# Kernel tuning notes

Hardware: AMD Instinct MI355X
Metric: run time of the kernel (lower is better)

## Reference

```python
import jax, jax.numpy as jnp
import numpy as np

# ---- static config (matches init_kwargs) ----
B, N, DIM = 1, 2048, 1024
H, KVH, D = 16, 8, 64
GQ = H // KVH                 # grouped queries per kv head
WS = 64                       # sliding window size (causal, exact)
CBS, STRIDE = 32, 16          # compress block size / sliding stride
SEL_BLK, NSEL, NMEM = 32, 4, 1
NCB = N // STRIDE             # num compressed blocks (128)
NFB = N // SEL_BLK            # num fine blocks (64)
NCPF = SEL_BLK // STRIDE      # compressed blocks per fine block (2)
HID = CBS * D                 # compress MLP hidden (expand factor 1.0)
SCALE = D ** -0.5
THETA = 10000.0
NEG = -jnp.finfo(jnp.float32).max


def setup_inputs():
    key = jax.random.key(0)
    ks = jax.random.split(key, 16)
    s = 0.02
    r = lambda i, shape: jax.random.normal(ks[i], shape, jnp.float32) * s
    return {
        "inp": jax.random.normal(ks[0], (B, N, DIM), jnp.float32),
        "norm_g": jnp.ones((DIM,), jnp.float32),
        "Wqkv": r(1, (DIM, (H + 2 * KVH) * D)),
        "mem_kv": r(2, (2, KVH, NMEM, D)),
        "k_pos": r(3, (KVH, CBS, D)),
        "v_pos": r(4, (KVH, CBS, D)),
        "kW1": r(5, (CBS * D, HID)), "kb1": jnp.zeros((HID,), jnp.float32),
        "kW2": r(6, (HID, D)), "kb2": jnp.zeros((D,), jnp.float32),
        "vW1": r(7, (CBS * D, HID)), "vb1": jnp.zeros((HID,), jnp.float32),
        "vW2": r(8, (HID, D)), "vb2": jnp.zeros((D,), jnp.float32),
        "combW": r(9, (DIM, 3 * H)),
        "combB": jnp.tile(jnp.array([-2.0, -2.0, 2.0], jnp.float32), H),
        "Wout": r(10, (H * D, DIM)),
    }


def _rope(t):
    # lucidrains rotary-embedding-torch: interleaved adjacent-pair rotation
    inv_freq = 1.0 / (THETA ** (jnp.arange(0, D, 2, dtype=jnp.float32) / D))
    ang = jnp.arange(N, dtype=jnp.float32)[:, None] * inv_freq        # [N, D/2]
    cos = jnp.repeat(jnp.cos(ang), 2, axis=-1)                        # [N, D]
    sin = jnp.repeat(jnp.sin(ang), 2, axis=-1)
    t2 = t.reshape(*t.shape[:-1], D // 2, 2)
    rot = jnp.stack([-t2[..., 1], t2[..., 0]], axis=-1).reshape(t.shape)
    return t * cos + rot * sin


def _forward(inp, norm_g, Wqkv, mem_kv, k_pos, v_pos,
             kW1, kb1, kW2, kb2, vW1, vb1, vW2, vb2,
             combW, combB, Wout):
    # RMSNorm
    x = inp * jax.lax.rsqrt(jnp.mean(inp * inp, -1, keepdims=True)
                            + jnp.finfo(inp.dtype).eps) * norm_g
    qkv = x @ Wqkv
    q, k, v = jnp.split(qkv, [H * D, H * D + KVH * D], axis=-1)
    q = q.reshape(B, N, H, D).transpose(0, 2, 1, 3)      # b h n d
    k = k.reshape(B, N, KVH, D).transpose(0, 2, 1, 3)    # b kvh n d
    v = v.reshape(B, N, KVH, D).transpose(0, 2, 1, 3)

    # ---- compressed branch (overlapping windows, left zero pad) ----
    overlap = CBS - STRIDE
    kp = jnp.pad(k, ((0, 0), (0, 0), (overlap, 0), (0, 0)))
    vp = jnp.pad(v, ((0, 0), (0, 0), (overlap, 0), (0, 0)))
    widx = jnp.arange(NCB)[:, None] * STRIDE + jnp.arange(CBS)[None, :]  # [NCB, CBS]
    kw = kp[:, :, widx] + k_pos[None, :, None]   # b kvh w cbs d
    vw = vp[:, :, widx] + v_pos[None, :, None]

    def cmlp(t, W1, b1, W2, b2):
        t = t.reshape(B, KVH, NCB, CBS * D)
        return jax.nn.relu(t @ W1 + b1) @ W2 + b2       # b kvh w d

    ck = cmlp(kw, kW1, kb1, kW2, kb2)
    cv = cmlp(vw, vW1, vb1, vW2, vb2)
    ck = jnp.concatenate([jnp.broadcast_to(mem_kv[0], (B, KVH, NMEM, D)), ck], 2)
    cv = jnp.concatenate([jnp.broadcast_to(mem_kv[1], (B, KVH, NMEM, D)), cv], 2)

    qg = q.reshape(B, KVH, GQ, N, D)
    csim = jnp.einsum('bhgid,bhjd->bhgij', qg, ck) * SCALE   # no mask (cmask=None)
    cattn = jax.nn.softmax(csim, -1)
    cout = jnp.einsum('bhgij,bhjd->bhgid', cattn, cv).reshape(B, H, N, D)

    # rotary AFTER compressed attention (as in source)
    rq, rk = _rope(q), _rope(k)

    # ---- importance scores -> top-k fine block selection ----
    imp = csim[..., NMEM:].mean(2)                          # b kvh n NCB (share grouped q)
    imp = imp.reshape(B, KVH, N, NFB, NCPF).mean(-1)        # mean-pool to fine blocks
    q_blk = jnp.arange(N) // SEL_BLK
    diag = q_blk[:, None] == jnp.arange(NFB)[None, :]
    imp = jnp.where(diag[None, None], NEG, imp)             # mask own (diagonal) block
    imp = jax.nn.softmax(jnp.pad(imp, ((0, 0),) * 3 + ((1, 0),),
                                 constant_values=-1000.0), -1)[..., 1:]
    sel_val, sel_idx = jax.lax.top_k(imp, NSEL)             # b kvh n NSEL

    # ---- fine (block-selected) attention ----
    own = jnp.broadcast_to(q_blk[None, None, :, None], (B, KVH, N, 1))
    sel_idx = jnp.concatenate([sel_idx, own], -1)           # append own block
    fmask = jnp.repeat((sel_val > 1e-10)[..., None], SEL_BLK, -1)  # b kvh n NSEL blk
    causal_row = jnp.tril(jnp.ones((SEL_BLK, SEL_BLK), bool))[jnp.arange(N) % SEL_BLK]
    causal = jnp.broadcast_to(causal_row[None, None, :, None, :],
                              (B, KVH, N, 1, SEL_BLK))
    fmask = jnp.concatenate([fmask, causal], 3).reshape(B, KVH, N, (NSEL + 1) * SEL_BLK)

    fk_blocks = rk.reshape(B, KVH, NFB, SEL_BLK, D)
    fv_blocks = v.reshape(B, KVH, NFB, SEL_BLK, D)
    gather = jax.vmap(jax.vmap(lambda blocks, idx: blocks[idx]))  # over b, kvh
    fk = gather(fk_blocks, sel_idx).reshape(B, KVH, N, (NSEL + 1) * SEL_BLK, D)
    fv = gather(fv_blocks, sel_idx).reshape(B, KVH, N, (NSEL + 1) * SEL_BLK, D)

    rqg = rq.reshape(B, KVH, GQ, N, D)
    fsim = jnp.einsum('bhgid,bhijd->bhgij', rqg, fk) * SCALE
    fsim = jnp.where(fmask[:, :, None], fsim, NEG / 10)
    fattn = jax.nn.softmax(fsim, -1)
    fout = jnp.einsum('bhgij,bhijd->bhgid', fattn, fv).reshape(B, H, N, D)

    # ---- sliding window (causal, exact window size WS) ----
    NW = N // WS
    kp2 = jnp.pad(rk, ((0, 0), (0, 0), (WS, 0), (0, 0)))
    vp2 = jnp.pad(v, ((0, 0), (0, 0), (WS, 0), (0, 0)))
    kidx = jnp.arange(NW)[:, None] * WS + jnp.arange(2 * WS)[None, :]
    kwin = kp2[:, :, kidx]                                  # b kvh nw 2ws d
    vwin = vp2[:, :, kidx]
    qwin = rqg.reshape(B, KVH, GQ, NW, WS, D)
    ssim = jnp.einsum('bhgwid,bhwjd->bhgwij', qwin, kwin) * SCALE
    i = jnp.arange(WS)[:, None]
    j = jnp.arange(2 * WS)[None, :]
    diff = i - (j - WS)
    local_ok = (diff >= 0) & (diff < WS)                    # [WS, 2WS]
    keypos = jnp.arange(NW)[:, None, None] * WS + (jnp.arange(2 * WS) - WS)[None, None, :]
    smask = local_ok[None] & (keypos >= 0)                  # [NW, WS, 2WS]
    ssim = jnp.where(smask[None, None, None], ssim, NEG)
    sattn = jax.nn.softmax(ssim, -1)
    sout = jnp.einsum('bhgwij,bhwjd->bhgwid', sattn, vwin).reshape(B, H, N, D)

    # ---- learned strategy combination (compressed, fine, sliding) ----
    gates = jax.nn.sigmoid(x @ combW + combB).reshape(B, N, H, 3).transpose(0, 2, 1, 3)
    out = gates[..., 0:1] * cout + gates[..., 1:2] * fout + gates[..., 2:3] * sout
    out = out.transpose(0, 2, 1, 3).reshape(B, N, H * D) @ Wout
    return out


def reference(inp, norm_g, Wqkv, mem_kv, k_pos, v_pos,
              kW1, kb1, kW2, kb2, vW1, vb1, vW2, vb2,
              combW, combB, Wout):
    return _forward(inp, norm_g, Wqkv, mem_kv, k_pos, v_pos,
                    kW1, kb1, kW2, kb2, vW1, vb1, vW2, vb2,
                    combW, combB, Wout)
```

## Files before the change

kernel.cpp:

```cpp
#include <hip/hip_runtime.h>
#include <hip/hip_bf16.h>

#define NTOK 2048
#define DIM 1024
#define NH 16
#define KVH 8
#define GQ 2
#define HD 64
#define WS 64
#define CBS 32
#define STRIDE 16
#define SEL_BLK 32
#define NSEL 4
#define NMEM 1
#define NCB 128
#define NFB 64
#define HIDN 2048
#define SCALE 0.125f
#define NEGF (-3.4028234663852886e38f)
#define NEG10F (-3.4028234663852886e37f)

typedef __attribute__((ext_vector_type(8))) short bf16x8;
typedef __attribute__((ext_vector_type(4))) float f32x4;

__device__ __forceinline__ float bflo(unsigned u) { return __uint_as_float(u << 16); }
__device__ __forceinline__ float bfhi(unsigned u) { return __uint_as_float(u & 0xffff0000u); }
__device__ __forceinline__ void dot8(const float4& qa, const float4& qb, uint4 a, float& s) {
    s += qa.x * bflo(a.x) + qa.y * bfhi(a.x) + qa.z * bflo(a.y) + qa.w * bfhi(a.y) +
         qb.x * bflo(a.z) + qb.y * bfhi(a.z) + qb.z * bflo(a.w) + qb.w * bfhi(a.w);
}

__device__ __forceinline__ void gload_lds16(const void* g, void* l) {
    __builtin_amdgcn_global_load_lds((const __attribute__((address_space(1))) unsigned*)g,
                                     (__attribute__((address_space(3))) unsigned*)l, 16, 0, 0);
}

__device__ __forceinline__ void rms_body(const float* __restrict__ inp,
                                         const float* __restrict__ g,
                                         float* __restrict__ x,
                                         __hip_bfloat16* __restrict__ xb, int n) {
    const float* row = inp + (size_t)n * DIM;
    float ss = 0.f;
    for (int c = threadIdx.x; c < DIM; c += 256) { float v = row[c]; ss += v * v; }
    __shared__ float red[4];
    for (int o = 32; o; o >>= 1) ss += __shfl_down(ss, o, 64);
    if ((threadIdx.x & 63) == 0) red[threadIdx.x >> 6] = ss;
    __syncthreads();
    if (threadIdx.x == 0) red[0] = red[0] + red[1] + red[2] + red[3];
    __syncthreads();
    float rs = 1.0f / sqrtf(red[0] / (float)DIM + 1.1920928955078125e-07f);
    float* xr = x + (size_t)n * DIM;
    __hip_bfloat16* xbr = xb + (size_t)n * DIM;
    for (int c = threadIdx.x; c < DIM; c += 256) {
        float v = row[c] * rs * g[c];
        xr[c] = v;
        xbr[c] = __float2bfloat16(v);
    }
}

__device__ __forceinline__ void transpose_body(const float* __restrict__ B,
                                               __hip_bfloat16* __restrict__ Bt,
                                               int K, int N, int bx, int by) {
    __shared__ float tile[32][33];
    int n0 = bx * 32, k0 = by * 32;
    int x = threadIdx.x & 31, y = threadIdx.x >> 5;
    for (int i = 0; i < 4; i++) {
        int k = k0 + y + 8 * i, n = n0 + x;
        tile[y + 8 * i][x] = (k < K && n < N) ? B[(size_t)k * N + n] : 0.f;
    }
    __syncthreads();
    for (int i = 0; i < 4; i++) {
        int n = n0 + y + 8 * i, k = k0 + x;
        if (n < N && k < K) Bt[(size_t)n * K + k] = __float2bfloat16(tile[x][y + 8 * i]);
    }
}

__global__ __launch_bounds__(256) void pre_kernel(
    const float* inp, const float* norm_g, float* x, __hip_bfloat16* xb,
    const float* Wqkv, __hip_bfloat16* Wqkvt,
    const float* kW1, __hip_bfloat16* kW1t,
    const float* vW1, __hip_bfloat16* vW1t,
    const float* Wout, __hip_bfloat16* Woutt,
    const float* combW, __hip_bfloat16* combWt,
    const float* kW2, __hip_bfloat16* kW2t,
    const float* vW2, __hip_bfloat16* vW2t,
    const float* combB, float* gatesb,
    const float* kb2, float* ckraw,
    const float* vb2, float* cvraw) {
    int b = blockIdx.x;
    if (b < 2048) { rms_body(inp, norm_g, x, xb, b); return; }
    b -= 2048;
    if (b < 2048) { transpose_body(Wqkv, Wqkvt, 1024, 2048, b % 64, b / 64); return; }
    b -= 2048;
    if (b < 4096) { transpose_body(kW1, kW1t, 2048, 2048, b % 64, b / 64); return; }
    b -= 4096;
    if (b < 4096) { transpose_body(vW1, vW1t, 2048, 2048, b % 64, b / 64); return; }
    b -= 4096;
    if (b < 1024) { transpose_body(Wout, Woutt, 1024, 1024, b % 32, b / 32); return; }
    b -= 1024;
    if (b < 64) { transpose_body(combW, combWt, 1024, 48, b % 2, b / 2); return; }
    b -= 64;
    if (b < 128) { transpose_body(kW2, kW2t, 2048, 64, b % 2, b / 2); return; }
    b -= 128;
    if (b < 128) { transpose_body(vW2, vW2t, 2048, 64, b % 2, b / 2); return; }
    b -= 128;
    if (b < 384) {
        int idx = b * 256 + threadIdx.x;
        if (idx < 2048 * 48) gatesb[idx] = combB[idx % 48];
        return;
    }
    b -= 384;
    {
// ... 86 lines not shown
        mfma_gemm_body<1, 1>(A1, Bt1, bias1, C1, M, N, K, blockIdx.x, blockIdx.y);
}

__device__ __forceinline__ void skgemm_body(const __hip_bfloat16* __restrict__ A,
                                            const __hip_bfloat16* __restrict__ Bt,
                                            float* __restrict__ C,
                                            int M, int Nout, int K, int by, int bz, int nz) {
    __shared__ __align__(16) short As2[128 * 32];
    __shared__ __align__(16) short Bs2[64 * 32];
    int tid = threadIdx.x;
    int lane = tid & 63, wave = tid >> 6;
    int m0 = by * 128;
    int wm = wave * 32;
    int kchunk = K / nz;
    int kbase = bz * kchunk;
    f32x4 acc[2][4];
    for (int r = 0; r < 2; r++)
        for (int c = 0; c < 4; c++) acc[r][c] = (f32x4){0.f, 0.f, 0.f, 0.f};

    int ra = tid >> 2, kc = (tid & 3) * 8;
    int rb = ra < Nout ? ra : Nout - 1;
    for (int k0 = kbase; k0 < kbase + kchunk; k0 += 32) {
        __syncthreads();
        gload_lds16(A + (size_t)(m0 + ra) * K + k0 + kc, &As2[ra * 32 + kc]);
        gload_lds16(A + (size_t)(m0 + ra + 64) * K + k0 + kc, &As2[(ra + 64) * 32 + kc]);
        gload_lds16(Bt + (size_t)rb * K + k0 + kc, &Bs2[ra * 32 + kc]);
        __syncthreads();
        bf16x8 af[2], bfr[4];
#pragma unroll
        for (int r = 0; r < 2; r++)
            af[r] = *(const bf16x8*)&As2[(wm + r * 16 + (lane & 15)) * 32 + (lane >> 4) * 8];
#pragma unroll
        for (int c = 0; c < 4; c++)
            bfr[c] = *(const bf16x8*)&Bs2[(c * 16 + (lane & 15)) * 32 + (lane >> 4) * 8];
#pragma unroll
        for (int r = 0; r < 2; r++)
#pragma unroll
            for (int c = 0; c < 4; c++)
                acc[r][c] = __builtin_amdgcn_mfma_f32_16x16x32_bf16(af[r], bfr[c], acc[r][c], 0, 0, 0);
    }
    for (int r = 0; r < 2; r++) {
        int grow = m0 + wm + r * 16 + (lane >> 4) * 4;
        for (int c = 0; c < 4; c++) {
            int gcol = c * 16 + (lane & 15);
            if (gcol >= Nout) continue;
#pragma unroll
            for (int v = 0; v < 4; v++)
                atomicAdd(&C[(size_t)(grow + v) * Nout + gcol], acc[r][c][v]);
        }
    }
}

__global__ __launch_bounds__(256) void qkv_gates_kernel(const __hip_bfloat16* xb,
                                                        const __hip_bfloat16* Wqkvt,
                                                        float* qkv,
                                                        const __hip_bfloat16* combWt,
                                                        float* gatesb) {
    int b = blockIdx.x;
    if (b < 256) {
        mfma_gemm_body<0, 0>(xb, Wqkvt, nullptr, qkv, 2048, 2048, 1024, b & 15, b >> 4);
    } else {
        int s = b - 256;
        skgemm_body(xb, combWt, gatesb, 2048, 48, 1024, s & 15, s >> 4, 4);
    }
}

__global__ __launch_bounds__(256) void skgemm_pair(const __hip_bfloat16* A0,
                                                   const __hip_bfloat16* A1,
                                                   const __hip_bfloat16* Bt0,
                                                   const __hip_bfloat16* Bt1,
                                                   float* C0, float* C1,
                                                   int M, int Nout, int K) {
    if (blockIdx.x == 0)
        skgemm_body(A0, Bt0, C0, M, Nout, K, blockIdx.y, blockIdx.z, gridDim.z);
    else
        skgemm_body(A1, Bt1, C1, M, Nout, K, blockIdx.y, blockIdx.z, gridDim.z);
}

__global__ __launch_bounds__(256) void winrope_kernel(const float* __restrict__ qkv,
                                                      const float* __restrict__ k_pos,
                                                      const float* __restrict__ v_pos,
                                                      __hip_bfloat16* __restrict__ kwflat,
                                                      __hip_bfloat16* __restrict__ vwflat,
                                                      float* __restrict__ rq,
                                                      __hip_bfloat16* __restrict__ rk,
                                                      __hip_bfloat16* __restrict__ vt) {
    int b = blockIdx.x;
    int t = threadIdx.x;
    if (b < 4096) {
        size_t total = (size_t)(KVH * NCB) * HIDN;
        for (size_t e = (size_t)b * 256 + t; e < total; e += (size_t)4096 * 256) {
            int r = (int)(e >> 11);
            int c = (int)(e & 2047);
            int j = c >> 6, d = c & 63;
            int h = r >> 7, i = r & 127;
            int p = i * STRIDE + j - (CBS - STRIDE);
            float kb = k_pos[((size_t)h * CBS + j) * HD + d];
            float vb = v_pos[((size_t)h * CBS + j) * HD + d];
            float kv = 0.f, vv = 0.f;
            if (p >= 0) {
                kv = qkv[(size_t)p * 2048 + 1024 + h * HD + d];
                vv = qkv[(size_t)p * 2048 + 1536 + h * HD + d];
            }
            kwflat[e] = __float2bfloat16(kv + kb);
            vwflat[e] = __float2bfloat16(vv + vb);
        }
        return;
    }
    int n = b - 4096;
    for (int idx = t; idx < NH * 32; idx += 256) {
        int h = idx >> 5, f = idx & 31;
        float inv = exp2f((float)f * -0.41524101186092f);
        float ang = (float)n * inv;
        float cc = cosf(ang), ssn = sinf(ang);
        float a = qkv[(size_t)n * 2048 + h * HD + 2 * f];
        float bq = qkv[(size_t)n * 2048 + h * HD + 2 * f + 1];
        float* o = rq + ((size_t)h * NTOK + n) * HD + 2 * f;
        o[0] = a * cc - bq * ssn;
        o[1] = bq * cc + a * ssn;
    }
    for (int idx = t; idx < KVH * 32; idx += 256) {
        int h = idx >> 5, f = idx & 31;
        float inv = exp2f((float)f * -0.41524101186092f);
        float ang = (float)n * inv;
        float cc = cosf(ang), ssn = sinf(ang);
        float a = qkv[(size_t)n * 2048 + 1024 + h * HD + 2 * f];
        float bq = qkv[(size_t)n * 2048 + 1024 + h * HD + 2 * f + 1];
        __hip_bfloat16* o = rk + ((size_t)h * NTOK + n) * HD + 2 * f;
        o[0] = __float2bfloat16(a * cc - bq * ssn);
        o[1] = __float2bfloat16(bq * cc + a * ssn);
    }
    for (int idx = t; idx < KVH * HD; idx += 256) {
        int h = idx >> 6, d = idx & 63;
        vt[((size_t)h * NTOK + n) * HD + d] =
            __float2bfloat16(qkv[(size_t)n * 2048 + 1536 + h * HD + d]);
    }
}

__global__ __launch_bounds__(256) void cattn2_kernel(const float* __restrict__ qkv,
                                                     const float* __restrict__ ckraw,
                                                     const float* __restrict__ cvraw,
                                                     const float* __restrict__ memkv,
                                                     float* __restrict__ cout,
                                                     int* __restrict__ selidx,
                                                     int* __restrict__ selmask) {
    int h = blockIdx.x >> 6;
    int i0 = (blockIdx.x & 63) * 32;
    int t = threadIdx.x;
    __shared__ float qs[64][68];
    __shared__ float sc[64][132];
    __shared__ float scratch[32 * 68];
    __shared__ float memk[64], memv[64];

    for (int idx = t; idx < 4096; idx += 256) {
        int row = idx >> 6, d = idx & 63;
        int g = row >> 5, qi = row & 31;
        qs[row][d] = qkv[(size_t)(i0 + qi) * 2048 + (h * 2 + g) * 64 + d];
    }
    if (t < 64) { memk[t] = memkv[h * 64 + t]; memv[t] = memkv[(8 + h) * 64 + t]; }
    __syncthreads();
    if (t < 64) {
        float s = 0.f;
        for (int d = 0; d < 64; d++) s += qs[t][d] * memk[d];
        sc[t][0] = s * SCALE;
    }
    int rg = t >> 3, kg = t & 7;
    for (int c = 0; c < 4; c++) {
        __syncthreads();
        for (int idx = t; idx < 2048; idx += 256) {
            int jj = idx >> 6, d = idx & 63;
            scratch[jj * 68 + d] = ckraw[((size_t)h * 128 + c * 32 + jj) * 64 + d];
        }
        __syncthreads();
        float a0[4] = {}, a1[4] = {};
        for (int d = 0; d < 64; d += 4) {
            float4 q0 = *(const float4*)&qs[rg * 2][d];
            float4 q1 = *(const float4*)&qs[rg * 2 + 1][d];
#pragma unroll
            for (int kk = 0; kk < 4; kk++) {
                float4 kv = *(const float4*)&scratch[(kg + kk * 8) * 68 + d];
                a0[kk] += q0.x * kv.x + q0.y * kv.y + q0.z * kv.z + q0.w * kv.w;
                a1[kk] += q1.x * kv.x + q1.y * kv.y + q1.z * kv.z + q1.w * kv.w;
            }
        }
#pragma unroll
        for (int kk = 0; kk < 4; kk++) {
            sc[rg * 2][1 + c * 32 + kg + kk * 8] = a0[kk] * SCALE;
            sc[rg * 2 + 1][1 + c * 32 + kg + kk * 8] = a1[kk] * SCALE;
        }
    }
    __syncthreads();
    for (int idx = t; idx < 2048; idx += 256) {
        int qi = idx >> 6, fb = idx & 63;
        float v = 0.25f * (sc[qi][1 + 2 * fb] + sc[qi][2 + 2 * fb] +
                           sc[32 + qi][1 + 2 * fb] + sc[32 + qi][2 + 2 * fb]);
        if (fb == ((i0 + qi) >> 5)) v = NEGF;
        scratch[qi * 66 + fb] = v;
    }
    __syncthreads();
    if (t < 32) {
        float* row = &scratch[t * 66];
        float m = -1000.f;
        for (int j = 0; j < 64; j++) m = fmaxf(m, row[j]);
        float den = __expf(-1000.f - m);
        for (int j = 0; j < 64; j++) den += __expf(row[j] - m);
        float invd = 1.f / den;
        unsigned long long taken = 0ull;
        int mk = 0;
        size_t base = ((size_t)h * NTOK + i0 + t) * 5;
        for (int p = 0; p < NSEL; p++) {
            float bv = NEGF;
            int bi = 0;
            for (int j = 0; j < 64; j++) {
                if (!((taken >> j) & 1ull) && row[j] > bv) { bv = row[j]; bi = j; }
            }
            taken |= 1ull << bi;
            selidx[base + p] = bi;
            if (__expf(bv - m) * invd > 1e-10f) mk |= 1 << p;
        }
        selidx[base + 4] = (i0 + t) >> 5;
        selmask[h * NTOK + i0 + t] = mk;
    } else if (t >= 64 && t < 128) {
        int r = t - 64;
        float m = NEGF;
        for (int j = 0; j < 129; j++) m = fmaxf(m, sc[r][j]);
        float den = 0.f;
        for (int j = 0; j < 129; j++) { float e = __expf(sc[r][j] - m); sc[r][j] = e; den += e; }
        float inv = 1.f / den;
        for (int j = 0; j < 129; j++) sc[r][j] *= inv;
    }
    __syncthreads();
    int dg = t & 7;
    float o0[8], o1[8];
    {
        float p0 = sc[rg * 2][0], p1 = sc[rg * 2 + 1][0];
#pragma unroll
        for (int dd = 0; dd < 8; dd++) {
            float v = memv[dg + dd * 8];
            o0[dd] = p0 * v;
            o1[dd] = p1 * v;
        }
    }
    for (int c = 0; c < 4; c++) {
        __syncthreads();
        for (int idx = t; idx < 2048; idx += 256) {
            int jj = idx >> 6, d = idx & 63;
            scratch[jj * 68 + d] = cvraw[((size_t)h * 128 + c * 32 + jj) * 64 + d];
        }
        __syncthreads();
        for (int jj = 0; jj < 32; jj++) {
            float p0 = sc[rg * 2][1 + c * 32 + jj];
            float p1 = sc[rg * 2 + 1][1 + c * 32 + jj];
#pragma unroll
            for (int dd = 0; dd < 8; dd++) {
                float v = scratch[jj * 68 + dg + dd * 8];
                o0[dd] += p0 * v;
                o1[dd] += p1 * v;
            }
        }
    }
    {
        int row = rg * 2;
        int g = row >> 5, qi = row & 31;
        int g2 = (row + 1) >> 5, qi2 = (row + 1) & 31;
#pragma unroll
        for (int dd = 0; dd < 8; dd++) {
            cout[(((size_t)(h * 2 + g)) * NTOK + i0 + qi) * 64 + dd * 8 + dg] = o0[dd];
            cout[(((size_t)(h * 2 + g2)) * NTOK + i0 + qi2) * 64 + dd * 8 + dg] = o1[dd];
        }
    }
}

__global__ __launch_bounds__(256) void attn_fused3_kernel(const float* __restrict__ rq,
                                                          const __hip_bfloat16* __restrict__ rk,
                                                          const __hip_bfloat16* __restrict__ vt,
                                                          const int* __restrict__ selidx,
                                                          const int* __restrict__ selmask,
                                                          float* __restrict__ fout,
                                                          float* __restrict__ sout) {
    int tid = threadIdx.x;
    int ws = tid >> 6, lane = tid & 63;
    __shared__ float pbuf[4][448];
    float* pf0 = pbuf[ws];
    float* pf1 = pf0 + 160;
    float* ps0 = pf0 + 320;
    float* ps1 = pf0 + 384;

    int kq = lane >> 2, c = lane & 3;
    int kv8 = lane >> 3, c8 = lane & 7;
    int wid = blockIdx.x * 4 + ws;
    int h = wid >> 11, i = wid & 2047;

    size_t sbase = ((size_t)h * NTOK + i) * 5;
    int selr[5];
#pragma unroll
    for (int s = 0; s < 5; s++) selr[s] = selidx[sbase + s];
    int mk = selmask[h * NTOK + i];

    const float* q0p = rq + ((size_t)(h * 2 + 0) * NTOK + i) * 64 + c * 16;
    const float* q1p = rq + ((size_t)(h * 2 + 1) * NTOK + i) * 64 + c * 16;
    float4 q0[4], q1[4];
#pragma unroll
    for (int u = 0; u < 4; u++) {
        q0[u] = *(const float4*)(q0p + u * 4);
        q1[u] = *(const float4*)(q1p + u * 4);
    }
    int iq = i & 31;

#pragma unroll
    for (int kt = 0; kt < 10; kt++) {
        int slot = kt >> 1;
        int blk = selr[slot];
        int key = kt * 16 + kq;
        int jj = key & 31;
        int kpos = blk * 32 + jj;
        bool valid = (slot < 4) ? (((mk >> slot) & 1) != 0) : (jj <= iq);
        const __hip_bfloat16* kr = rk + ((size_t)h * NTOK + kpos) * 64 + c * 16;
        float s0 = 0.f, s1 = 0.f;
        uint4 a = *(const uint4*)(kr);
        uint4 b = *(const uint4*)(kr + 8);
        dot8(q0[0], q0[1], a, s0); dot8(q0[2], q0[3], b, s0);
        dot8(q1[0], q1[1], a, s1); dot8(q1[2], q1[3], b, s1);
        s0 += __shfl_xor(s0, 1); s0 += __shfl_xor(s0, 2);
        s1 += __shfl_xor(s1, 1); s1 += __shfl_xor(s1, 2);
        if (c == 0) {
            pf0[key] = valid ? s0 * SCALE : NEG10F;
            pf1[key] = valid ? s1 * SCALE : NEG10F;
        }
    }
#pragma unroll
    for (int kt = 0; kt < 4; kt++) {
        int koff = kt * 16 + kq;
        int kpos = i - 63 + koff;
        bool valid = kpos >= 0;
        int kcl = valid ? kpos : 0;
        const __hip_bfloat16* kr = rk + ((size_t)h * NTOK + kcl) * 64 + c * 16;
        float s0 = 0.f, s1 = 0.f;
        uint4 a = *(const uint4*)(kr);
        uint4 b = *(const uint4*)(kr + 8);
        dot8(q0[0], q0[1], a, s0); dot8(q0[2], q0[3], b, s0);
        dot8(q1[0], q1[1], a, s1); dot8(q1[2], q1[3], b, s1);
        s0 += __shfl_xor(s0, 1); s0 += __shfl_xor(s0, 2);
        s1 += __shfl_xor(s1, 1); s1 += __shfl_xor(s1, 2);
        if (c == 0) {
            ps0[koff] = valid ? s0 * SCALE : NEG10F;
            ps1[koff] = valid ? s1 * SCALE : NEG10F;
        }
    }
    {
        float a0 = pf0[lane], b0 = pf0[lane + 64];
        float c0 = (lane < 32) ? pf0[lane + 128] : NEG10F;
        float a1 = pf1[lane], b1 = pf1[lane + 64];
        float c1 = (lane < 32) ? pf1[lane + 128] : NEG10F;
        float m0 = fmaxf(fmaxf(a0, b0), c0);
        float m1 = fmaxf(fmaxf(a1, b1), c1);
#pragma unroll
        for (int o = 1; o < 64; o <<= 1) {
            m0 = fmaxf(m0, __shfl_xor(m0, o));
            m1 = fmaxf(m1, __shfl_xor(m1, o));
        }
        float ea0 = __expf(a0 - m0), eb0 = __expf(b0 - m0), ec0 = (lane < 32) ? __expf(c0 - m0) : 0.f;
        float ea1 = __expf(a1 - m1), eb1 = __expf(b1 - m1), ec1 = (lane < 32) ? __expf(c1 - m1) : 0.f;
        float d0 = ea0 + eb0 + ec0;
        float d1 = ea1 + eb1 + ec1;
#pragma unroll
        for (int o = 1; o < 64; o <<= 1) {
            d0 += __shfl_xor(d0, o);
            d1 += __shfl_xor(d1, o);
        }
        float inv0 = 1.f / d0, inv1 = 1.f / d1;
        pf0[lane] = ea0 * inv0; pf0[lane + 64] = eb0 * inv0;
        pf1[lane] = ea1 * inv1; pf1[lane + 64] = eb1 * inv1;
        if (lane < 32) { pf0[lane + 128] = ec0 * inv0; pf1[lane + 128] = ec1 * inv1; }
    }
    {
        float a0 = ps0[lane], a1 = ps1[lane];
        float m0 = a0, m1 = a1;
#pragma unroll
        for (int o = 1; o < 64; o <<= 1) {
            m0 = fmaxf(m0, __shfl_xor(m0, o));
            m1 = fmaxf(m1, __shfl_xor(m1, o));
        }
        float e0 = __expf(a0 - m0), e1 = __expf(a1 - m1);
        float d0 = e0, d1 = e1;
#pragma unroll
        for (int o = 1; o < 64; o <<= 1) {
            d0 += __shfl_xor(d0, o);
            d1 += __shfl_xor(d1, o);
        }
        ps0[lane] = e0 / d0;
        ps1[lane] = e1 / d1;
    }
    {
        float o0[8] = {}, o1[8] = {};
#pragma unroll
        for (int slot = 0; slot < 5; slot++) {
            const __hip_bfloat16* vbase = vt + ((size_t)h * NTOK + selr[slot] * 32) * 64;
#pragma unroll
            for (int pass = 0; pass < 4; pass++) {
                int j = pass * 8 + kv8;
                uint4 v = *(const uint4*)(vbase + j * 64 + c8 * 8);
                float pa = pf0[slot * 32 + j], pb = pf1[slot * 32 + j];
                float e0 = bflo(v.x), e1 = bfhi(v.x), e2 = bflo(v.y), e3 = bfhi(v.y);
                float e4 = bflo(v.z), e5 = bfhi(v.z), e6 = bflo(v.w), e7 = bfhi(v.w);
                o0[0] = fmaf(pa, e0, o0[0]); o0[1] = fmaf(pa, e1, o0[1]);
                o0[2] = fmaf(pa, e2, o0[2]); o0[3] = fmaf(pa, e3, o0[3]);
                o0[4] = fmaf(pa, e4, o0[4]); o0[5] = fmaf(pa, e5, o0[5]);
                o0[6] = fmaf(pa, e6, o0[6]); o0[7] = fmaf(pa, e7, o0[7]);
                o1[0] = fmaf(pb, e0, o1[0]); o1[1] = fmaf(pb, e1, o1[1]);
                o1[2] = fmaf(pb, e2, o1[2]); o1[3] = fmaf(pb, e3, o1[3]);
                o1[4] = fmaf(pb, e4, o1[4]); o1[5] = fmaf(pb, e5, o1[5]);
                o1[6] = fmaf(pb, e6, o1[6]); o1[7] = fmaf(pb, e7, o1[7]);
            }
        }
#pragma unroll
        for (int o = 8; o <= 32; o <<= 1)
#pragma unroll
            for (int d = 0; d < 8; d++) {
                o0[d] += __shfl_xor(o0[d], o);
                o1[d] += __shfl_xor(o1[d], o);
            }
        if (kv8 == 0) {
            float* f0 = fout + ((size_t)(h * 2 + 0) * NTOK + i) * 64 + c8 * 8;
            float* f1 = fout + ((size_t)(h * 2 + 1) * NTOK + i) * 64 + c8 * 8;
            *(float4*)(f0) = (float4){o0[0], o0[1], o0[2], o0[3]};
            *(float4*)(f0 + 4) = (float4){o0[4], o0[5], o0[6], o0[7]};
            *(float4*)(f1) = (float4){o1[0], o1[1], o1[2], o1[3]};
            *(float4*)(f1 + 4) = (float4){o1[4], o1[5], o1[6], o1[7]};
        }
    }
    {
        float o0[8] = {}, o1[8] = {};
#pragma unroll
        for (int pass = 0; pass < 8; pass++) {
            int j = pass * 8 + kv8;
            int kpos = i - 63 + j;
            int kcl = kpos >= 0 ? kpos : 0;
            uint4 v = *(const uint4*)(vt + ((size_t)h * NTOK + kcl) * 64 + c8 * 8);
            float pa = ps0[j], pb = ps1[j];
            float e0 = bflo(v.x), e1 = bfhi(v.x), e2 = bflo(v.y), e3 = bfhi(v.y);
            float e4 = bflo(v.z), e5 = bfhi(v.z), e6 = bflo(v.w), e7 = bfhi(v.w);
            o0[0] = fmaf(pa, e0, o0[0]); o0[1] = fmaf(pa, e1, o0[1]);
            o0[2] = fmaf(pa, e2, o0[2]); o0[3] = fmaf(pa, e3, o0[3]);
            o0[4] = fmaf(pa, e4, o0[4]); o0[5] = fmaf(pa, e5, o0[5]);
            o0[6] = fmaf(pa, e6, o0[6]); o0[7] = fmaf(pa, e7, o0[7]);
            o1[0] = fmaf(pb, e0, o1[0]); o1[1] = fmaf(pb, e1, o1[1]);
            o1[2] = fmaf(pb, e2, o1[2]); o1[3] = fmaf(pb, e3, o1[3]);
            o1[4] = fmaf(pb, e4, o1[4]); o1[5] = fmaf(pb, e5, o1[5]);
            o1[6] = fmaf(pb, e6, o1[6]); o1[7] = fmaf(pb, e7, o1[7]);
        }
#pragma unroll
        for (int o = 8; o <= 32; o <<= 1)
#pragma unroll
            for (int d = 0; d < 8; d++) {
                o0[d] += __shfl_xor(o0[d], o);
                o1[d] += __shfl_xor(o1[d], o);
            }
        if (kv8 == 0) {
            float* s0p = sout + ((size_t)(h * 2 + 0) * NTOK + i) * 64 + c8 * 8;
            float* s1p = sout + ((size_t)(h * 2 + 1) * NTOK + i) * 64 + c8 * 8;
            *(float4*)(s0p) = (float4){o0[0], o0[1], o0[2], o0[3]};
            *(float4*)(s0p + 4) = (float4){o0[4], o0[5], o0[6], o0[7]};
            *(float4*)(s1p) = (float4){o1[0], o1[1], o1[2], o1[3]};
            *(float4*)(s1p + 4) = (float4){o1[4], o1[5], o1[6], o1[7]};
        }
    }
}

__global__ __launch_bounds__(256) void combine_kernel(const float* __restrict__ gateslin,
                                                      const float* __restrict__ cout,
                                                      const float* __restrict__ fout,
                                                      const float* __restrict__ sout,
                                                      __hip_bfloat16* __restrict__ att) {
    int n = blockIdx.x;
    for (int c = threadIdx.x; c < NH * HD; c += 256) {
        int hd = c >> 6, d = c & 63;
        float g0 = 1.f / (1.f + expf(-gateslin[(size_t)n * (NH * 3) + hd * 3 + 0]));
        float g1 = 1.f / (1.f + expf(-gateslin[(size_t)n * (NH * 3) + hd * 3 + 1]));
        float g2 = 1.f / (1.f + expf(-gateslin[(size_t)n * (NH * 3) + hd * 3 + 2]));
        size_t o = ((size_t)hd * NTOK + n) * HD + d;
        att[(size_t)n * (NH * HD) + c] =
            __float2bfloat16(g0 * cout[o] + g1 * fout[o] + g2 * sout[o]);
    }
}

extern "C" void kernel_launch(void* const* d_in, const int* in_sizes, int n_in,
                              void* d_out, int out_size, void* d_ws, size_t ws_size,
                              hipStream_t stream) {
    const float* inp    = (const float*)d_in[0];
    const float* norm_g = (const float*)d_in[1];
    const float* Wqkv   = (const float*)d_in[2];
    const float* mem_kv = (const float*)d_in[3];
    const float* k_pos  = (const float*)d_in[4];
    const float* v_pos  = (const float*)d_in[5];
    const float* kW1    = (const float*)d_in[6];
    const float* kb1    = (const float*)d_in[7];
    const float* kW2    = (const float*)d_in[8];
    const float* kb2    = (const float*)d_in[9];
    const float* vW1    = (const float*)d_in[10];
    const float* vb1    = (const float*)d_in[11];
    const float* vW2    = (const float*)d_in[12];
    const float* vb2    = (const float*)d_in[13];
    const float* combW  = (const float*)d_in[14];
    const float* combB  = (const float*)d_in[15];
    const float* Wout   = (const float*)d_in[16];
    float* out = (float*)d_out;

    char* base = (char*)d_ws;
    size_t off = 0;
    auto alloc = [&](size_t bytes) {
        void* p = base + off;
        off += (bytes + 255) & ~(size_t)255;
        return p;
    };
    float* x            = (float*)alloc((size_t)NTOK * DIM * 4);
    __hip_bfloat16* xb  = (__hip_bfloat16*)alloc((size_t)NTOK * DIM * 2);
    float* qkv          = (float*)alloc((size_t)NTOK * 2048 * 4);
    __hip_bfloat16* Wqkvt = (__hip_bfloat16*)alloc((size_t)2048 * 1024 * 2);
    __hip_bfloat16* kW1t  = (__hip_bfloat16*)alloc((size_t)2048 * 2048 * 2);
    __hip_bfloat16* vW1t  = (__hip_bfloat16*)alloc((size_t)2048 * 2048 * 2);
    __hip_bfloat16* Woutt = (__hip_bfloat16*)alloc((size_t)1024 * 1024 * 2);
    __hip_bfloat16* combWt = (__hip_bfloat16*)alloc((size_t)48 * 1024 * 2);
    __hip_bfloat16* kW2t  = (__hip_bfloat16*)alloc((size_t)64 * 2048 * 2);
    __hip_bfloat16* vW2t  = (__hip_bfloat16*)alloc((size_t)64 * 2048 * 2);
    __hip_bfloat16* kwflat = (__hip_bfloat16*)alloc((size_t)KVH * NCB * HIDN * 2);
    __hip_bfloat16* vwflat = (__hip_bfloat16*)alloc((size_t)KVH * NCB * HIDN * 2);
    __hip_bfloat16* hidkb = (__hip_bfloat16*)alloc((size_t)KVH * NCB * HIDN * 2);
    __hip_bfloat16* hidvb = (__hip_bfloat16*)alloc((size_t)KVH * NCB * HIDN * 2);
    float* ckraw        = (float*)alloc((size_t)KVH * NCB * HD * 4);
    float* cvraw        = (float*)alloc((size_t)KVH * NCB * HD * 4);
    float* rq           = (float*)alloc((size_t)NH * NTOK * HD * 4);
    __hip_bfloat16* rk  = (__hip_bfloat16*)alloc((size_t)KVH * NTOK * HD * 2);
    __hip_bfloat16* vt  = (__hip_bfloat16*)alloc((size_t)KVH * NTOK * HD * 2);
    float* coutb        = (float*)alloc((size_t)NH * NTOK * HD * 4);
    float* foutb        = (float*)alloc((size_t)NH * NTOK * HD * 4);
    float* soutb        = (float*)alloc((size_t)NH * NTOK * HD * 4);
    float* gatesb       = (float*)alloc((size_t)NTOK * NH * 3 * 4);
    __hip_bfloat16* attb = (__hip_bfloat16*)alloc((size_t)NTOK * DIM * 2);
    int* selidx         = (int*)alloc((size_t)KVH * NTOK * 5 * 4);
    int* selmask        = (int*)alloc((size_t)KVH * NTOK * 4);
    (void)ws_size; (void)in_sizes; (void)n_in; (void)out_size;

    pre_kernel<<<PRE_BLOCKS, 256, 0, stream>>>(inp, norm_g, x, xb,
                                               Wqkv, Wqkvt, kW1, kW1t, vW1, vW1t,
                                               Wout, Woutt, combW, combWt,
                                               kW2, kW2t, vW2, vW2t,
                                               combB, gatesb, kb2, ckraw, vb2, cvraw);
    qkv_gates_kernel<<<320, 256, 0, stream>>>(xb, Wqkvt, qkv, combWt, gatesb);
    winrope_kernel<<<4096 + 2048, 256, 0, stream>>>(qkv, k_pos, v_pos, kwflat, vwflat,
                                                    rq, rk, vt);
    mfma_gemm_pair<<<dim3(16, 8, 2), 256, 0, stream>>>(kwflat, vwflat, kW1t, vW1t,
                                                       kb1, vb1, hidkb, hidvb,
                                                       1024, 2048, 2048);
    skgemm_pair<<<dim3(2, 8, 8), 256, 0, stream>>>(hidkb, hidvb, kW2t, vW2t,
                                                   ckraw, cvraw, 1024, 64, 2048);
    cattn2_kernel<<<KVH * (NTOK / 32), 256, 0, stream>>>(qkv, ckraw, cvraw, mem_kv,
                                                         coutb, selidx, selmask);
    attn_fused3_kernel<<<4096, 256, 0, stream>>>(rq, rk, vt, selidx, selmask,
                                                 foutb, soutb);
    combine_kernel<<<NTOK, 256, 0, stream>>>(gatesb, coutb, foutb, soutb, attb);
    mfma_gemm<0, 0><<<dim3(8, 16), 256, 0, stream>>>(attb, Woutt, nullptr, out, 2048, 1024, 1024);
}
```

Before: 382.5 us.

## Move fine and sliding attention onto MFMA with bf16 queries and transposed V

Replaces the scalar dot-product attention kernel with one that computes QK^T and PV for the selected fine blocks and the sliding window using 16x16x32 bf16 MFMA instructions. Queries are now stored as bf16, and a new transpose kernel produces a d-major copy of V so PV can be fed to MFMA. Probabilities are packed to bf16 in LDS. Only 2 of the 16 MFMA columns are real queries, so much of each MFMA is wasted. The change also adds an extra launch and lowers the precision of queries and probabilities.

```diff
diff --git a/kernel.cpp b/kernel.cpp
--- a/kernel.cpp
+++ b/kernel.cpp
@@ -25,9 +25,9 @@
 
 __device__ __forceinline__ float bflo(unsigned u) { return __uint_as_float(u << 16); }
 __device__ __forceinline__ float bfhi(unsigned u) { return __uint_as_float(u & 0xffff0000u); }
-__device__ __forceinline__ void dot8(const float4& qa, const float4& qb, uint4 a, float& s) {
-    s += qa.x * bflo(a.x) + qa.y * bfhi(a.x) + qa.z * bflo(a.y) + qa.w * bfhi(a.y) +
-         qb.x * bflo(a.z) + qb.y * bfhi(a.z) + qb.z * bflo(a.w) + qb.w * bfhi(a.w);
+__device__ __forceinline__ unsigned pack2bf(float a, float b) {
+    return ((unsigned)__bfloat16_as_ushort(__float2bfloat16(b)) << 16) |
+           (unsigned)__bfloat16_as_ushort(__float2bfloat16(a));
 }
 
 __device__ __forceinline__ void gload_lds16(const void* g, void* l) {
@@ -280,7 +280,7 @@
                                                       const float* __restrict__ v_pos,
                                                       __hip_bfloat16* __restrict__ kwflat,
                                                       __hip_bfloat16* __restrict__ vwflat,
-                                                      float* __restrict__ rq,
+                                                      __hip_bfloat16* __restrict__ rqb,
                                                       __hip_bfloat16* __restrict__ rk,
                                                       __hip_bfloat16* __restrict__ vt) {
     int b = blockIdx.x;
@@ -313,9 +313,9 @@
         float cc = cosf(ang), ssn = sinf(ang);
         float a = qkv[(size_t)n * 2048 + h * HD + 2 * f];
         float bq = qkv[(size_t)n * 2048 + h * HD + 2 * f + 1];
-        float* o = rq + ((size_t)h * NTOK + n) * HD + 2 * f;
-        o[0] = a * cc - bq * ssn;
-        o[1] = bq * cc + a * ssn;
+        __hip_bfloat16* o = rqb + ((size_t)h * NTOK + n) * HD + 2 * f;
+        o[0] = __float2bfloat16(a * cc - bq * ssn);
+        o[1] = __float2bfloat16(bq * cc + a * ssn);
     }
     for (int idx = t; idx < KVH * 32; idx += 256) {
         int h = idx >> 5, f = idx & 31;
@@ -332,6 +332,28 @@
         int h = idx >> 6, d = idx & 63;
         vt[((size_t)h * NTOK + n) * HD + d] =
             __float2bfloat16(qkv[(size_t)n * 2048 + 1536 + h * HD + d]);
+    }
+}
+
+__global__ __launch_bounds__(256) void vtrans_kernel(const __hip_bfloat16* __restrict__ vt,
+                                                     __hip_bfloat16* __restrict__ vtt) {
+    __shared__ unsigned short tile[64][68];
+    int h = blockIdx.x >> 5;
+    int t0 = (blockIdx.x & 31) * 64;
+    int tid = threadIdx.x;
+    for (int idx = tid; idx < 512; idx += 256) {
+        int row = idx >> 3, dblk = idx & 7;
+        uint4 v = *(const uint4*)(vt + ((size_t)h * NTOK + t0 + row) * 64 + dblk * 8);
+        unsigned* dst = (unsigned*)&tile[row][dblk * 8];
+        dst[0] = v.x; dst[1] = v.y; dst[2] = v.z; dst[3] = v.w;
+    }
+    __syncthreads();
+    for (int idx = tid; idx < 512; idx += 256) {
+        int d = idx >> 3, tblk = idx & 7;
+        union { uint4 v; unsigned short s[8]; } w;
+#pragma unroll
+        for (int u = 0; u < 8; u++) w.s[u] = tile[tblk * 8 + u][d];
+        *(uint4*)(vtt + ((size_t)(h * 64 + d)) * NTOK + t0 + tblk * 8) = w.v;
     }
 }
 
@@ -469,198 +491,174 @@
     }
 }
 
-__global__ __launch_bounds__(256) void attn_fused3_kernel(const float* __restrict__ rq,
-                                                          const __hip_bfloat16* __restrict__ rk,
-                                                          const __hip_bfloat16* __restrict__ vt,
-                                                          const int* __restrict__ selidx,
-                                                          const int* __restrict__ selmask,
-                                                          float* __restrict__ fout,
-                                                          float* __restrict__ sout) {
+__global__ __launch_bounds__(256) void attn_mfma_kernel(
+    const __hip_bfloat16* __restrict__ rqb,
+    const __hip_bfloat16* __restrict__ rk,
+    const __hip_bfloat16* __restrict__ vtt,
+    const int* __restrict__ selidx,
+    const int* __restrict__ selmask,
+    float* __restrict__ fout,
+    float* __restrict__ sout) {
     int tid = threadIdx.x;
     int ws = tid >> 6, lane = tid & 63;
-    __shared__ float pbuf[4][448];
-    float* pf0 = pbuf[ws];
-    float* pf1 = pf0 + 160;
-    float* ps0 = pf0 + 320;
-    float* ps1 = pf0 + 384;
-
-    int kq = lane >> 2, c = lane & 3;
-    int kv8 = lane >> 3, c8 = lane & 7;
+    int g = lane >> 4, qh = lane & 15, qsel = qh & 1;
     int wid = blockIdx.x * 4 + ws;
     int h = wid >> 11, i = wid & 2047;
 
+    __shared__ __align__(16) unsigned short Pf[4][2][160];
+    __shared__ __align__(16) unsigned short Ps[4][2][96];
+
     size_t sbase = ((size_t)h * NTOK + i) * 5;
     int selr[5];
 #pragma unroll
     for (int s = 0; s < 5; s++) selr[s] = selidx[sbase + s];
     int mk = selmask[h * NTOK + i];
-
-    const float* q0p = rq + ((size_t)(h * 2 + 0) * NTOK + i) * 64 + c * 16;
-    const float* q1p = rq + ((size_t)(h * 2 + 1) * NTOK + i) * 64 + c * 16;
-    float4 q0[4], q1[4];
-#pragma unroll
-    for (int u = 0; u < 4; u++) {
-        q0[u] = *(const float4*)(q0p + u * 4);
-        q1[u] = *(const float4*)(q1p + u * 4);
-    }
     int iq = i & 31;
-
-#pragma unroll
-    for (int kt = 0; kt < 10; kt++) {
-        int slot = kt >> 1;
-        int blk = selr[slot];
-        int key = kt * 16 + kq;
-        int jj = key & 31;
-        int kpos = blk * 32 + jj;
-        bool valid = (slot < 4) ? (((mk >> slot) & 1) != 0) : (jj <= iq);
-        const __hip_bfloat16* kr = rk + ((size_t)h * NTOK + kpos) * 64 + c * 16;
-        float s0 = 0.f, s1 = 0.f;
-        uint4 a = *(const uint4*)(kr);
-        uint4 b = *(const uint4*)(kr + 8);
-        dot8(q0[0], q0[1], a, s0); dot8(q0[2], q0[3], b, s0);
-        dot8(q1[0], q1[1], a, s1); dot8(q1[2], q1[3], b, s1);
-        s0 += __shfl_xor(s0, 1); s0 += __shfl_xor(s0, 2);
-        s1 += __shfl_xor(s1, 1); s1 += __shfl_xor(s1, 2);
-        if (c == 0) {
-            pf0[key] = valid ? s0 * SCALE : NEG10F;
-            pf1[key] = valid ? s1 * SCALE : NEG10F;
-        }
-    }
-#pragma unroll
-    for (int kt = 0; kt < 4; kt++) {
-        int koff = kt * 16 + kq;
-        int kpos = i - 63 + koff;
-        bool valid = kpos >= 0;
-        int kcl = valid ? kpos : 0;
-        const __hip_bfloat16* kr = rk + ((size_t)h * NTOK + kcl) * 64 + c * 16;
-        float s0 = 0.f, s1 = 0.f;
-        uint4 a = *(const uint4*)(kr);
-        uint4 b = *(const uint4*)(kr + 8);
-        dot8(q0[0], q0[1], a, s0); dot8(q0[2], q0[3], b, s0);
-        dot8(q1[0], q1[1], a, s1); dot8(q1[2], q1[3], b, s1);
-        s0 += __shfl_xor(s0, 1); s0 += __shfl_xor(s0, 2);
-        s1 += __shfl_xor(s1, 1); s1 += __shfl_xor(s1, 2);
-        if (c == 0) {
-            ps0[koff] = valid ? s0 * SCALE : NEG10F;
-            ps1[koff] = valid ? s1 * SCALE : NEG10F;
+    int cb = (i - 63) & ~31;
+
+    const __hip_bfloat16* qrow = rqb + ((size_t)(h * 2 + qsel) * NTOK + i) * 64;
+    bf16x8 bq0 = *(const bf16x8*)(qrow + g * 8);
+    bf16x8 bq1 = *(const bf16x8*)(qrow + 32 + g * 8);
+
+    const __hip_bfloat16* krow = rk + (size_t)h * NTOK * 64;
+
+    f32x4 sf[5][2];
+#pragma unroll
+    for (int c = 0; c < 5; c++) {
+        int base = selr[c] * 32;
+#pragma unroll
+        for (int kf = 0; kf < 2; kf++) {
+            const __hip_bfloat16* kr = krow + (size_t)(base + kf * 16 + qh) * 64;
+            bf16x8 a0 = *(const bf16x8*)(kr + g * 8);
+            bf16x8 a1 = *(const bf16x8*)(kr + 32 + g * 8);
+            f32x4 acc = (f32x4){0.f, 0.f, 0.f, 0.f};
+            acc = __builtin_amdgcn_mfma_f32_16x16x32_bf16(a0, bq0, acc, 0, 0, 0);
+            acc = __builtin_amdgcn_mfma_f32_16x16x32_bf16(a1, bq1, acc, 0, 0, 0);
+            sf[c][kf] = acc;
         }
     }
     {
-        float a0 = pf0[lane], b0 = pf0[lane + 64];
-        float c0 = (lane < 32) ? pf0[lane + 128] : NEG10F;
-        float a1 = pf1[lane], b1 = pf1[lane + 64];
-        float c1 = (lane < 32) ? pf1[lane + 128] : NEG10F;
-        float m0 = fmaxf(fmaxf(a0, b0), c0);
-        float m1 = fmaxf(fmaxf(a1, b1), c1);
-#pragma unroll
-        for (int o = 1; o < 64; o <<= 1) {
-            m0 = fmaxf(m0, __shfl_xor(m0, o));
-            m1 = fmaxf(m1, __shfl_xor(m1, o));
-        }
-        float ea0 = __expf(a0 - m0), eb0 = __expf(b0 - m0), ec0 = (lane < 32) ? __expf(c0 - m0) : 0.f;
-        float ea1 = __expf(a1 - m1), eb1 = __expf(b1 - m1), ec1 = (lane < 32) ? __expf(c1 - m1) : 0.f;
-        float d0 = ea0 + eb0 + ec0;
-        float d1 = ea1 + eb1 + ec1;
-#pragma unroll
-        for (int o = 1; o < 64; o <<= 1) {
-            d0 += __shfl_xor(d0, o);
-            d1 += __shfl_xor(d1, o);
-        }
-        float inv0 = 1.f / d0, inv1 = 1.f / d1;
-        pf0[lane] = ea0 * inv0; pf0[lane + 64] = eb0 * inv0;
-        pf1[lane] = ea1 * inv1; pf1[lane + 64] = eb1 * inv1;
-        if (lane < 32) { pf0[lane + 128] = ec0 * inv0; pf1[lane + 128] = ec1 * inv1; }
+        float m = NEG10F;
+#pragma unroll
+        for (int c = 0; c < 5; c++)
+#pragma unroll
+            for (int kf = 0; kf < 2; kf++)
+#pragma unroll
+                for (int v = 0; v < 4; v++) {
+                    int loc = kf * 16 + g * 4 + v;
+                    bool valid = (c < 4) ? (((mk >> c) & 1) != 0) : (loc <= iq);
+                    float z = valid ? sf[c][kf][v] * SCALE : NEG10F;
+                    sf[c][kf][v] = z;
+                    m = fmaxf(m, z);
+                }
+        m = fmaxf(m, __shfl_xor(m, 16));
+        m = fmaxf(m, __shfl_xor(m, 32));
+        float den = 0.f;
+#pragma unroll
+        for (int c = 0; c < 5; c++)
+#pragma unroll
+            for (int kf = 0; kf < 2; kf++)
+#pragma unroll
+                for (int v = 0; v < 4; v++) {
+                    float e = __expf(sf[c][kf][v] - m);
+                    sf[c][kf][v] = e;
+                    den += e;
+                }
+        den += __shfl_xor(den, 16);
+        den += __shfl_xor(den, 32);
+        float inv = 1.f / den;
+        if (qh < 2) {
+#pragma unroll
+            for (int c = 0; c < 5; c++)
+#pragma unroll
+                for (int kf = 0; kf < 2; kf++) {
+                    unsigned* dst = (unsigned*)&Pf[ws][qh][c * 32 + kf * 16 + g * 4];
+                    dst[0] = pack2bf(sf[c][kf][0] * inv, sf[c][kf][1] * inv);
+                    dst[1] = pack2bf(sf[c][kf][2] * inv, sf[c][kf][3] * inv);
+                }
+        }
+    }
+    f32x4 ss[3][2];
+#pragma unroll
+    for (int c = 0; c < 3; c++) {
+        int base = cb + c * 32;
+#pragma unroll
+        for (int kf = 0; kf < 2; kf++) {
+            int row = base + kf * 16 + qh;
+            int rcl = min(max(row, 0), NTOK - 1);
+            const __hip_bfloat16* kr = krow + (size_t)rcl * 64;
+            bf16x8 a0 = *(const bf16x8*)(kr + g * 8);
+            bf16x8 a1 = *(const bf16x8*)(kr + 32 + g * 8);
+            f32x4 acc = (f32x4){0.f, 0.f, 0.f, 0.f};
+            acc = __builtin_amdgcn_mfma_f32_16x16x32_bf16(a0, bq0, acc, 0, 0, 0);
+            acc = __builtin_amdgcn_mfma_f32_16x16x32_bf16(a1, bq1, acc, 0, 0, 0);
+            ss[c][kf] = acc;
+        }
     }
     {
-        float a0 = ps0[lane], a1 = ps1[lane];
-        float m0 = a0, m1 = a1;
-#pragma unroll
-        for (int o = 1; o < 64; o <<= 1) {
-            m0 = fmaxf(m0, __shfl_xor(m0, o));
-            m1 = fmaxf(m1, __shfl_xor(m1, o));
-        }
-        float e0 = __expf(a0 - m0), e1 = __expf(a1 - m1);
-        float d0 = e0, d1 = e1;
-#pragma unroll
-        for (int o = 1; o < 64; o <<= 1) {
-            d0 += __shfl_xor(d0, o);
-            d1 += __shfl_xor(d1, o);
-        }
-        ps0[lane] = e0 / d0;
-        ps1[lane] = e1 / d1;
-    }
-    {
-        float o0[8] = {}, o1[8] = {};
-#pragma unroll
-        for (int slot = 0; slot < 5; slot++) {
-            const __hip_bfloat16* vbase = vt + ((size_t)h * NTOK + selr[slot] * 32) * 64;
-#pragma unroll
-            for (int pass = 0; pass < 4; pass++) {
-                int j = pass * 8 + kv8;
-                uint4 v = *(const uint4*)(vbase + j * 64 + c8 * 8);
-                float pa = pf0[slot * 32 + j], pb = pf1[slot * 32 + j];
-                float e0 = bflo(v.x), e1 = bfhi(v.x), e2 = bflo(v.y), e3 = bfhi(v.y);
-                float e4 = bflo(v.z), e5 = bfhi(v.z), e6 = bflo(v.w), e7 = bfhi(v.w);
-                o0[0] = fmaf(pa, e0, o0[0]); o0[1] = fmaf(pa, e1, o0[1]);
-                o0[2] = fmaf(pa, e2, o0[2]); o0[3] = fmaf(pa, e3, o0[3]);
-                o0[4] = fmaf(pa, e4, o0[4]); o0[5] = fmaf(pa, e5, o0[5]);
-                o0[6] = fmaf(pa, e6, o0[6]); o0[7] = fmaf(pa, e7, o0[7]);
-                o1[0] = fmaf(pb, e0, o1[0]); o1[1] = fmaf(pb, e1, o1[1]);
-                o1[2] = fmaf(pb, e2, o1[2]); o1[3] = fmaf(pb, e3, o1[3]);
-                o1[4] = fmaf(pb, e4, o1[4]); o1[5] = fmaf(pb, e5, o1[5]);
-                o1[6] = fmaf(pb, e6, o1[6]); o1[7] = fmaf(pb, e7, o1[7]);
-            }
-        }
-#pragma unroll
-        for (int o = 8; o <= 32; o <<= 1)
-#pragma unroll
-            for (int d = 0; d < 8; d++) {
-                o0[d] += __shfl_xor(o0[d], o);
-                o1[d] += __shfl_xor(o1[d], o);
-            }
-        if (kv8 == 0) {
-            float* f0 = fout + ((size_t)(h * 2 + 0) * NTOK + i) * 64 + c8 * 8;
-            float* f1 = fout + ((size_t)(h * 2 + 1) * NTOK + i) * 64 + c8 * 8;
-            *(float4*)(f0) = (float4){o0[0], o0[1], o0[2], o0[3]};
-            *(float4*)(f0 + 4) = (float4){o0[4], o0[5], o0[6], o0[7]};
-            *(float4*)(f1) = (float4){o1[0], o1[1], o1[2], o1[3]};
-            *(float4*)(f1 + 4) = (float4){o1[4], o1[5], o1[6], o1[7]};
-        }
-    }
-    {
-        float o0[8] = {}, o1[8] = {};
-#pragma unroll
-        for (int pass = 0; pass < 8; pass++) {
-            int j = pass * 8 + kv8;
-            int kpos = i - 63 + j;
-            int kcl = kpos >= 0 ? kpos : 0;
-            uint4 v = *(const uint4*)(vt + ((size_t)h * NTOK + kcl) * 64 + c8 * 8);
-            float pa = ps0[j], pb = ps1[j];
-            float e0 = bflo(v.x), e1 = bfhi(v.x), e2 = bflo(v.y), e3 = bfhi(v.y);
-            float e4 = bflo(v.z), e5 = bfhi(v.z), e6 = bflo(v.w), e7 = bfhi(v.w);
-            o0[0] = fmaf(pa, e0, o0[0]); o0[1] = fmaf(pa, e1, o0[1]);
-            o0[2] = fmaf(pa, e2, o0[2]); o0[3] = fmaf(pa, e3, o0[3]);
-            o0[4] = fmaf(pa, e4, o0[4]); o0[5] = fmaf(pa, e5, o0[5]);
-            o0[6] = fmaf(pa, e6, o0[6]); o0[7] = fmaf(pa, e7, o0[7]);
-            o1[0] = fmaf(pb, e0, o1[0]); o1[1] = fmaf(pb, e1, o1[1]);
-            o1[2] = fmaf(pb, e2, o1[2]); o1[3] = fmaf(pb, e3, o1[3]);
-            o1[4] = fmaf(pb, e4, o1[4]); o1[5] = fmaf(pb, e5, o1[5]);
-            o1[6] = fmaf(pb, e6, o1[6]); o1[7] = fmaf(pb, e7, o1[7]);
-        }
-#pragma unroll
-        for (int o = 8; o <= 32; o <<= 1)
-#pragma unroll
-            for (int d = 0; d < 8; d++) {
-                o0[d] += __shfl_xor(o0[d], o);
-                o1[d] += __shfl_xor(o1[d], o);
-            }
-        if (kv8 == 0) {
-            float* s0p = sout + ((size_t)(h * 2 + 0) * NTOK + i) * 64 + c8 * 8;
-            float* s1p = sout + ((size_t)(h * 2 + 1) * NTOK + i) * 64 + c8 * 8;
-            *(float4*)(s0p) = (float4){o0[0], o0[1], o0[2], o0[3]};
-            *(float4*)(s0p + 4) = (float4){o0[4], o0[5], o0[6], o0[7]};
-            *(float4*)(s1p) = (float4){o1[0], o1[1], o1[2], o1[3]};
-            *(float4*)(s1p + 4) = (float4){o1[4], o1[5], o1[6], o1[7]};
+        float m = NEG10F;
+#pragma unroll
+        for (int c = 0; c < 3; c++)
+#pragma unroll
+            for (int kf = 0; kf < 2; kf++)
+#pragma unroll
+                for (int v = 0; v < 4; v++) {
+                    int pos = cb + c * 32 + kf * 16 + g * 4 + v;
+                    bool valid = (pos >= i - 63) && (pos <= i) && (pos >= 0);
+                    float z = valid ? ss[c][kf][v] * SCALE : NEG10F;
+                    ss[c][kf][v] = z;
+                    m = fmaxf(m, z);
+                }
+        m = fmaxf(m, __shfl_xor(m, 16));
+        m = fmaxf(m, __shfl_xor(m, 32));
+        float den = 0.f;
+#pragma unroll
+        for (int c = 0; c < 3; c++)
+#pragma unroll
+            for (int kf = 0; kf < 2; kf++)
+#pragma unroll
+                for (int v = 0; v < 4; v++) {
+                    float e = __expf(ss[c][kf][v] - m);
+                    ss[c][kf][v] = e;
+                    den += e;
+                }
+        den += __shfl_xor(den, 16);
+        den += __shfl_xor(den, 32);
+        float inv = 1.f / den;
+        if (qh < 2) {
+#pragma unroll
+            for (int c = 0; c < 3; c++)
+#pragma unroll
+                for (int kf = 0; kf < 2; kf++) {
+                    unsigned* dst = (unsigned*)&Ps[ws][qh][c * 32 + kf * 16 + g * 4];
+                    dst[0] = pack2bf(ss[c][kf][0] * inv, ss[c][kf][1] * inv);
+                    dst[1] = pack2bf(ss[c][kf][2] * inv, ss[c][kf][3] * inv);
+                }
+        }
+    }
+#pragma unroll
+    for (int df = 0; df < 4; df++) {
+        const __hip_bfloat16* vrow = vtt + (size_t)(h * 64 + df * 16 + qh) * NTOK;
+        f32x4 accF = (f32x4){0.f, 0.f, 0.f, 0.f};
+#pragma unroll
+        for (int c = 0; c < 5; c++) {
+            bf16x8 av = *(const bf16x8*)(vrow + selr[c] * 32 + g * 8);
+            bf16x8 bp = *(const bf16x8*)&Pf[ws][qsel][c * 32 + g * 8];
+            accF = __builtin_amdgcn_mfma_f32_16x16x32_bf16(av, bp, accF, 0, 0, 0);
+        }
+        f32x4 accS = (f32x4){0.f, 0.f, 0.f, 0.f};
+#pragma unroll
+        for (int c = 0; c < 3; c++) {
+            int t = min(max(cb + c * 32 + g * 8, 0), NTOK - 8);
+            bf16x8 av = *(const bf16x8*)(vrow + t);
+            bf16x8 bp = *(const bf16x8*)&Ps[ws][qsel][c * 32 + g * 8];
+            accS = __builtin_amdgcn_mfma_f32_16x16x32_bf16(av, bp, accS, 0, 0, 0);
+        }
+        if (qh < 2) {
+            float* fo = fout + ((size_t)(h * 2 + qh) * NTOK + i) * 64 + df * 16 + g * 4;
+            *(float4*)fo = (float4){accF[0], accF[1], accF[2], accF[3]};
+            float* so = sout + ((size_t)(h * 2 + qh) * NTOK + i) * 64 + df * 16 + g * 4;
+            *(float4*)so = (float4){accS[0], accS[1], accS[2], accS[3]};
         }
     }
 }
@@ -727,9 +725,10 @@
     __hip_bfloat16* hidvb = (__hip_bfloat16*)alloc((size_t)KVH * NCB * HIDN * 2);
     float* ckraw        = (float*)alloc((size_t)KVH * NCB * HD * 4);
     float* cvraw        = (float*)alloc((size_t)KVH * NCB * HD * 4);
-    float* rq           = (float*)alloc((size_t)NH * NTOK * HD * 4);
+    __hip_bfloat16* rqb = (__hip_bfloat16*)alloc((size_t)NH * NTOK * HD * 2);
     __hip_bfloat16* rk  = (__hip_bfloat16*)alloc((size_t)KVH * NTOK * HD * 2);
     __hip_bfloat16* vt  = (__hip_bfloat16*)alloc((size_t)KVH * NTOK * HD * 2);
+    __hip_bfloat16* vtt = (__hip_bfloat16*)alloc((size_t)KVH * HD * NTOK * 2);
     float* coutb        = (float*)alloc((size_t)NH * NTOK * HD * 4);
     float* foutb        = (float*)alloc((size_t)NH * NTOK * HD * 4);
     float* soutb        = (float*)alloc((size_t)NH * NTOK * HD * 4);
@@ -746,7 +745,8 @@
                                                combB, gatesb, kb2, ckraw, vb2, cvraw);
     qkv_gates_kernel<<<320, 256, 0, stream>>>(xb, Wqkvt, qkv, combWt, gatesb);
     winrope_kernel<<<4096 + 2048, 256, 0, stream>>>(qkv, k_pos, v_pos, kwflat, vwflat,
-                                                    rq, rk, vt);
+                                                    rqb, rk, vt);
+    vtrans_kernel<<<256, 256, 0, stream>>>(vt, vtt);
     mfma_gemm_pair<<<dim3(16, 8, 2), 256, 0, stream>>>(kwflat, vwflat, kW1t, vW1t,
                                                        kb1, vb1, hidkb, hidvb,
                                                        1024, 2048, 2048);
@@ -754,8 +754,8 @@
                                                    ckraw, cvraw, 1024, 64, 2048);
     cattn2_kernel<<<KVH * (NTOK / 32), 256, 0, stream>>>(qkv, ckraw, cvraw, mem_kv,
                                                          coutb, selidx, selmask);
-    attn_fused3_kernel<<<4096, 256, 0, stream>>>(rq, rk, vt, selidx, selmask,
-                                                 foutb, soutb);
+    attn_mfma_kernel<<<4096, 256, 0, stream>>>(rqb, rk, vtt, selidx, selmask,
+                                               foutb, soutb);
     combine_kernel<<<NTOK, 256, 0, stream>>>(gatesb, coutb, foutb, soutb, attb);
     mfma_gemm<0, 0><<<dim3(8, 16), 256, 0, stream>>>(attb, Woutt, nullptr, out, 2048, 1024, 1024);
 }
```

After: 427.1 us. 11.7% more time.
